# Kernel tuning notes

Measured on AMD Instinct MI355X. Metric: run time of the kernel, lower is better.

## Reference

```python
import jax, jax.numpy as jnp
import numpy as np

B, N, C, H = 2, 2048, 1024, 16
D = C // H
SCALE = 1.0 / np.sqrt(D)
MASK_VAL = -10000.0


def setup_inputs() -> dict:
    key = jax.random.key(0)
    k1, k2, k3 = jax.random.split(key, 3)
    hidden_state = jax.random.normal(k1, (B, N, C), dtype=jnp.float32)
    attention_mask = jax.random.randint(k2, (B, N), 0, 2) == 1  # True = padded
    # fused QKV projection weight, torch Linear convention: y = x @ W.T, W: [3C, C]
    W = jax.random.normal(k3, (3 * C, C), dtype=jnp.float32) * 0.02
    return {"hidden_state": hidden_state, "W": W, "attention_mask": attention_mask}


def reference(hidden_state, W, attention_mask):
    b, n, c = hidden_state.shape
    # fused QKV: [B,N,3C] -> [B,N,3,H,D] -> [3,B,H,N,D]
    wx = jnp.einsum('bnc,oc->bno', hidden_state, W).reshape(b, n, 3, H, D)
    wx = jnp.transpose(wx, (2, 0, 3, 1, 4))
    q, k, v = wx[0], wx[1], wx[2]
    scores = jnp.einsum('bhid,bhjd->bhij', q, k) * SCALE
    # construct_mask: pairwise OR of per-token padding mask, broadcast over heads
    m = attention_mask
    expanded = (m[:, None, :, None] | m[:, None, None, :])  # [B,1,N,N]
    scores = jnp.where(expanded, MASK_VAL, scores)
    scores = scores - jnp.max(scores, axis=-1, keepdims=True)
    att_weights = jax.nn.softmax(scores, axis=-1)
    # dropout_rate = 0.0 -> identity
    att = jnp.einsum('bhij,bhjd->bhid', att_weights, v)
    att = jnp.transpose(att, (0, 2, 1, 3)).reshape(b, n, c)
    return (att, att_weights)
```

## Files before the change

kernel.cpp:

```cpp
#include <hip/hip_runtime.h>


typedef unsigned short u16;
typedef __attribute__((ext_vector_type(8))) short bf16x8;
typedef __attribute__((ext_vector_type(4))) float f32x4;

#define B_ 2
#define N_ 2048
#define H_ 16
#define D_ 64
#define QKV_MAT 4194304
#define ATTW_OFF 4194304
#define OFF_MASK 25165824
#define OFF_FLAG 25182208
#define OFF_XB   25182464
#define OFF_WB   33571072

#define SCALE_L2 0.18033688011112042f
#define MASK_L2  -14426.950408889634f

__device__ __forceinline__ u16 f32_bf16(float f) {
  unsigned u = __float_as_uint(f);
  u += 0x7fffu + ((u >> 16) & 1u);
  return (u16)(u >> 16);
}
__device__ __forceinline__ float bf16_f32(unsigned h) {
  return __uint_as_float(h << 16);
}
__device__ __forceinline__ bf16x8 ld_frag(const u16* p) { return *(const bf16x8*)p; }

__device__ __forceinline__ void gld16(u16* l, const u16* g) {
  __builtin_amdgcn_global_load_lds(
      (const __attribute__((address_space(1))) void*)g,
      (__attribute__((address_space(3))) void*)l, 16, 0, 0);
}

__device__ __forceinline__ void bar_lgkm0() {
  __builtin_amdgcn_sched_barrier(0);
  asm volatile("s_waitcnt lgkmcnt(0)" ::: "memory");
  __builtin_amdgcn_s_barrier();
  __builtin_amdgcn_sched_barrier(0);
}
__device__ __forceinline__ void bar_vm4() {
  __builtin_amdgcn_sched_barrier(0);
  asm volatile("s_waitcnt vmcnt(4)" ::: "memory");
  __builtin_amdgcn_s_barrier();
  __builtin_amdgcn_sched_barrier(0);
}
__device__ __forceinline__ void bar_vm8() {
  __builtin_amdgcn_sched_barrier(0);
  asm volatile("s_waitcnt vmcnt(8)" ::: "memory");
  __builtin_amdgcn_s_barrier();
  __builtin_amdgcn_sched_barrier(0);
}

__global__ void detect_prep(const unsigned char* __restrict__ mraw,
                            const unsigned* __restrict__ X32,
                            int* __restrict__ flag) {
  __shared__ int votes, mflags;
  const int tid = threadIdx.x;
  if (tid == 0) { votes = 0; mflags = 0; }
  __syncthreads();
  int v = 0;
  for (int i = tid; i < 4096; i += 1024) {
    unsigned low = X32[i] & 0xFFFFu;
    unsigned e = (low >> 7) & 0xFFu;
    if (low == 0 || (e >= 80 && e <= 150)) v++;
  }
  atomicAdd(&votes, v);
  int fl = 0;
  for (int p = tid; p < B_ * N_; p += 1024) {
    unsigned char c = mraw[p];
    if (c > 1) fl |= 1;
    if (c && (p & 3) == 1) fl |= 4;
    if (c && (p & 3) != 0) fl |= 2;
    if (c && (p & 7) == 4) fl |= 8;
  }
  if (fl) atomicOr(&mflags, fl);
  __syncthreads();
  if (tid == 0) { flag[0] = (votes < 2600) ? 1 : 0; flag[1] = mflags; }
}

__global__ __launch_bounds__(256) void convert_in(const void* __restrict__ X,
                                                  const void* __restrict__ W,
                                                  const unsigned char* __restrict__ mraw,
                                                  u16* __restrict__ Xb, u16* __restrict__ Wb,
                                                  int* __restrict__ mout,
                                                  const int* __restrict__ flag) {
  const int f32m = flag[0];
  const int f = flag[1];
  const int gid = blockIdx.x * 256 + threadIdx.x;
  for (int i = gid; i < B_ * N_; i += gridDim.x * 256) {
    int m;
    if (f & 1) {
      if (f & 4) m = (((const u16*)mraw)[i] & 0x7FFFu) != 0;
      else       m = (((const unsigned*)mraw)[i] << 1) != 0;
    } else if (f & 2) m = mraw[i] != 0;
    else if (f & 8)   m = ((const int*)mraw)[i] != 0;
    else              m = ((const long long*)mraw)[i] != 0;
    mout[i] = m;
  }
  const int XC = (B_ * N_ * 1024) / 8;
  const int WC = (3072 * 1024) / 8;
  for (int idx = gid; idx < XC + WC; idx += gridDim.x * 256) {
    const void* src; u16* dst; int c;
    if (idx < XC) { c = idx; src = X; dst = Xb; }
    else          { c = idx - XC; src = W; dst = Wb; }
    if (f32m) {
      const float4* s = (const float4*)src;
      float4 a = s[c * 2], b = s[c * 2 + 1];
      unsigned p0 = (unsigned)f32_bf16(a.x) | ((unsigned)f32_bf16(a.y) << 16);
      unsigned p1 = (unsigned)f32_bf16(a.z) | ((unsigned)f32_bf16(a.w) << 16);
      unsigned p2 = (unsigned)f32_bf16(b.x) | ((unsigned)f32_bf16(b.y) << 16);
      unsigned p3 = (unsigned)f32_bf16(b.z) | ((unsigned)f32_bf16(b.w) << 16);
      ((uint4*)dst)[c] = make_uint4(p0, p1, p2, p3);
    } else {
      ((uint4*)dst)[c] = ((const uint4*)src)[c];
    }
  }
}

__global__ __launch_bounds__(256) void qkv_gemm(const u16* __restrict__ X,
                                                const u16* __restrict__ W,
                                                u16* __restrict__ qkv) {
  __shared__ u16 xs[128 * 64];
  __shared__ u16 wsh[128 * 64];
  const int tid = threadIdx.x;
  const int w = tid >> 6, l = tid & 63, quad = l >> 4, ln = l & 15;
  const int r0 = blockIdx.y * 128;
  const int o0 = blockIdx.x * 128;

  const f32x4 z4 = {0.f, 0.f, 0.f, 0.f};
  f32x4 acc[2][8];
#pragma unroll
  for (int rt = 0; rt < 2; rt++)
#pragma unroll
    for (int ct = 0; ct < 8; ct++) acc[rt][ct] = z4;

  for (int kc = 0; kc < 1024; kc += 64) {
#pragma unroll
    for (int ro = 0; ro < 4; ro++) {
      int q = ro * 256 + tid;
      int r = q >> 3, s = q & 7;
      int c = s ^ (r & 7);
      gld16(xs + q * 8, X + (size_t)(r0 + r) * 1024 + kc + c * 8);
      gld16(wsh + q * 8, W + (size_t)(o0 + r) * 1024 + kc + c * 8);
    }
    __syncthreads();
#pragma unroll
    for (int k2 = 0; k2 < 2; k2++) {
      bf16x8 af[2], bfr[8];
#pragma unroll
      for (int rt = 0; rt < 2; rt++) {
        int row = w * 32 + rt * 16 + ln;
        int slot = (k2 * 4 + quad) ^ (row & 7);
        af[rt] = ld_frag(xs + row * 64 + slot * 8);
      }
#pragma unroll
      for (int ct = 0; ct < 8; ct++) {
        int row = ct * 16 + ln;
        int slot = (k2 * 4 + quad) ^ (row & 7);
        bfr[ct] = ld_frag(wsh + row * 64 + slot * 8);
      }
#pragma unroll
      for (int rt = 0; rt < 2; rt++)
#pragma unroll
        for (int ct = 0; ct < 8; ct++)
          acc[rt][ct] = __builtin_amdgcn_mfma_f32_16x16x32_bf16(af[rt], bfr[ct], acc[rt][ct], 0, 0, 0);
    }
    __syncthreads();
  }

  const int b = r0 >> 11;
#pragma unroll
  for (int rt = 0; rt < 2; rt++) {
#pragma unroll
    for (int ct = 0; ct < 8; ct++) {
      int o = o0 + ct * 16 + ln;
      int sel = o >> 10;
      int h = (o >> 6) & 15;
      int d = o & 63;
      int nbase = (r0 & 2047) + w * 32 + rt * 16 + quad * 4;
      if (sel < 2) {
        size_t base = (size_t)sel * QKV_MAT + ((size_t)(b * 16 + h) * N_ + nbase) * D_ + d;
#pragma unroll
        for (int g = 0; g < 4; g++)
          qkv[base + (size_t)g * D_] = f32_bf16(acc[rt][ct][g]);
      } else {
        size_t base = 2 * (size_t)QKV_MAT + ((size_t)(b * 16 + h) * D_ + d) * N_ + nbase;
        unsigned lo = (unsigned)f32_bf16(acc[rt][ct][0]) | ((unsigned)f32_bf16(acc[rt][ct][1]) << 16);
        unsigned hi = (unsigned)f32_bf16(acc[rt][ct][2]) | ((unsigned)f32_bf16(acc[rt][ct][3]) << 16);
        *(uint2*)(qkv + base) = make_uint2(lo, hi);
      }
    }
  }
}

__global__ __launch_bounds__(256) void attn_kernel(const u16* __restrict__ qkv,
                                                   const int* __restrict__ mask,
                                                   void* __restrict__ outv,
                                                   const int* __restrict__ flag) {
  __shared__ u16 qs[128 * 64];
  __shared__ u16 ks[2][64 * 64];
  __shared__ u16 vs[2][64 * 64];
  __shared__ u16 ps[128 * 72];
  __shared__ float mrow[128];
  __shared__ float rlrow[128];

  const int of32 = __builtin_amdgcn_readfirstlane(flag[0]);
  u16* outh = (u16*)outv;
  float* outf = (float*)outv;

  const int tid = threadIdx.x;
  const int w = tid >> 6, l = tid & 63, quad = l >> 4, ln = l & 15;
  const int bh = blockIdx.x & 31;
  const int qt = blockIdx.x >> 5;
  const int b = bh >> 4, h = bh & 15;
  const int q0 = qt * 128;

  const u16* Qg = qkv + ((size_t)bh * N_ + q0) * D_;
  const u16* Kg = qkv + QKV_MAT + (size_t)bh * N_ * D_;
  const u16* Vg = qkv + 2 * (size_t)QKV_MAT + (size_t)bh * D_ * N_;
  const int* mb = mask + b * N_;
  const size_t attw_base = (size_t)ATTW_OFF + (size_t)bh * N_ * N_ + (size_t)q0 * N_;

#pragma unroll
  for (int ro = 0; ro < 4; ro++) {
    int q = ro * 256 + tid;
    int r = q >> 3, s = q & 7;
    int c = s ^ (r & 7);
    gld16(qs + q * 8, Qg + (size_t)r * D_ + c * 8);
  }
#pragma unroll
  for (int ro = 0; ro < 2; ro++) {
    int q = ro * 256 + tid;
    int r = q >> 3, s = q & 7;
    int c = s ^ (r & 7);
    gld16(ks[0] + q * 8, Kg + (size_t)r * D_ + c * 8);
  }
  int rowpad[2][4];
#pragma unroll
  for (int rt = 0; rt < 2; rt++)
#pragma unroll
    for (int g = 0; g < 4; g++)
      rowpad[rt][g] = mb[q0 + w * 32 + rt * 16 + quad * 4 + g];
  __syncthreads();

  bf16x8 qa[2][2];
#pragma unroll
  for (int rt = 0; rt < 2; rt++)
#pragma unroll
    for (int k2 = 0; k2 < 2; k2++) {
      int row = w * 32 + rt * 16 + ln;
      int slot = (k2 * 4 + quad) ^ (row & 7);
      qa[rt][k2] = ld_frag(qs + row * 64 + slot * 8);
    }

  float lsum[2][4] = {{0.f, 0.f, 0.f, 0.f}, {0.f, 0.f, 0.f, 0.f}};
  const f32x4 z4 = {0.f, 0.f, 0.f, 0.f};

  for (int kt = 0; kt < 32; kt++) {
    const int cur = kt & 1;
    if (kt < 31) {
#pragma unroll
      for (int ro = 0; ro < 2; ro++) {
        int q = ro * 256 + tid;
        int r = q >> 3, s = q & 7;
        int c = s ^ (r & 7);
        gld16(ks[cur ^ 1] + q * 8, Kg + (size_t)((kt + 1) * 64 + r) * D_ + c * 8);
      }
    }
    int cp[4];
#pragma unroll
    for (int ct = 0; ct < 4; ct++) cp[ct] = mb[kt * 64 + ct * 16 + ln];

    f32x4 sacc[2][4];
#pragma unroll
    for (int rt = 0; rt < 2; rt++)
#pragma unroll
      for (int ct = 0; ct < 4; ct++) sacc[rt][ct] = z4;
#pragma unroll
    for (int k2 = 0; k2 < 2; k2++) {
      bf16x8 kb[4];
#pragma unroll
      for (int ct = 0; ct < 4; ct++) {
        int row = ct * 16 + ln;
        int slot = (k2 * 4 + quad) ^ (row & 7);
        kb[ct] = ld_frag(ks[cur] + row * 64 + slot * 8);
      }
#pragma unroll
      for (int rt = 0; rt < 2; rt++)
#pragma unroll
        for (int ct = 0; ct < 4; ct++)
          sacc[rt][ct] = __builtin_amdgcn_mfma_f32_16x16x32_bf16(qa[rt][k2], kb[ct], sacc[rt][ct], 0, 0, 0);
    }
#pragma unroll
    for (int rt = 0; rt < 2; rt++)
#pragma unroll
      for (int g = 0; g < 4; g++) {
        float e = 0.f;
#pragma unroll
        for (int ct = 0; ct < 4; ct++) {
          float sv = sacc[rt][ct][g] * SCALE_L2;
          sv = (rowpad[rt][g] | cp[ct]) ? MASK_L2 : sv;
          e += __builtin_amdgcn_exp2f(sv);
        }
        lsum[rt][g] += e;
      }
    __syncthreads();
  }

#pragma unroll
  for (int ro = 0; ro < 2; ro++) {
    int q = ro * 256 + tid;
    int r = q >> 3, s = q & 7;
    int c = s ^ (r & 7);
    gld16(ks[0] + q * 8, Kg + (size_t)r * D_ + c * 8);
    gld16(vs[0] + q * 8, Vg + (size_t)r * N_ + c * 8);
  }

#pragma unroll
  for (int rt = 0; rt < 2; rt++)
#pragma unroll
    for (int g = 0; g < 4; g++) {
      float lv = lsum[rt][g];
      lv += __shfl_xor(lv, 1);
      lv += __shfl_xor(lv, 2);
      lv += __shfl_xor(lv, 4);
      lv += __shfl_xor(lv, 8);
      if (ln == 0) {
        int i = w * 32 + rt * 16 + quad * 4 + g;
        mrow[i] = rowpad[rt][g] ? MASK_L2 : 0.f;
        rlrow[i] = rowpad[rt][g] ? (1.f / 2048.f) : (1.f / lv);
      }
    }
  __syncthreads();

  bf16x8 qb[8][2];
  float mi[8], rli[8];
#pragma unroll
  for (int it = 0; it < 8; it++) {
    int row = it * 16 + ln;
#pragma unroll
    for (int k2 = 0; k2 < 2; k2++) {
      int slot = (k2 * 4 + quad) ^ (row & 7);
      qb[it][k2] = ld_frag(qs + row * 64 + slot * 8);
    }
    mi[it] = mrow[row];
    rli[it] = rlrow[row];
  }

  f32x4 oacc[2][4];
#pragma unroll
  for (int rt = 0; rt < 2; rt++)
#pragma unroll
    for (int dt = 0; dt < 4; dt++) oacc[rt][dt] = z4;

  for (int kt = 0; kt < 32; kt++) {
    const int cur = kt & 1;
    int cpj[4];
#pragma unroll
    for (int g = 0; g < 4; g++) cpj[g] = mb[kt * 64 + w * 16 + quad * 4 + g];

    bf16x8 ka[2];
#pragma unroll
    for (int k2 = 0; k2 < 2; k2++) {
      int row = w * 16 + ln;
      int slot = (k2 * 4 + quad) ^ (row & 7);
      ka[k2] = ld_frag(ks[cur] + row * 64 + slot * 8);
    }
#pragma unroll
    for (int it = 0; it < 8; it++) {
      f32x4 st = z4;
      st = __builtin_amdgcn_mfma_f32_16x16x32_bf16(ka[0], qb[it][0], st, 0, 0, 0);
      st = __builtin_amdgcn_mfma_f32_16x16x32_bf16(ka[1], qb[it][1], st, 0, 0, 0);
      bool rp = mi[it] < -5000.f;
      unsigned pk[4];
#pragma unroll
      for (int g = 0; g < 4; g++) {
        float sv = st[g] * SCALE_L2;
        sv = (cpj[g] || rp) ? MASK_L2 : sv;
        float p = __builtin_amdgcn_exp2f(sv - mi[it]) * rli[it];
        pk[g] = f32_bf16(p);
      }
      int iRow = it * 16 + ln;
      int jc = w * 16 + quad * 4;
      *(uint2*)(ps + iRow * 72 + jc) = make_uint2(pk[0] | (pk[1] << 16), pk[2] | (pk[3] << 16));
    }
    bar_lgkm0();

    if (kt < 31) {
#pragma unroll
      for (int ro = 0; ro < 2; ro++) {
        int q = ro * 256 + tid;
        int r = q >> 3, s = q & 7;
        int c = s ^ (r & 7);
        gld16(ks[cur ^ 1] + q * 8, Kg + (size_t)((kt + 1) * 64 + r) * D_ + c * 8);
        gld16(vs[cur ^ 1] + q * 8, Vg + (size_t)r * N_ + (kt + 1) * 64 + c * 8);
      }
    }

    if (!of32) {
#pragma unroll
      for (int ro = 0; ro < 4; ro++) {
        int q = ro * 256 + tid;
        int r = q >> 3, c = q & 7;
        uint4 v = *(const uint4*)(ps + r * 72 + c * 8);
        *(uint4*)(outh + attw_base + (size_t)r * N_ + kt * 64 + c * 8) = v;
      }
    } else {
#pragma unroll
      for (int ro = 0; ro < 8; ro++) {
        int q = ro * 256 + tid;
        int r = q >> 4, c4 = q & 15;
        uint2 v = *(const uint2*)(ps + r * 72 + c4 * 4);
        float4 o = make_float4(bf16_f32(v.x & 0xFFFFu), bf16_f32(v.x >> 16),
                               bf16_f32(v.y & 0xFFFFu), bf16_f32(v.y >> 16));
        *(float4*)(outf + attw_base + (size_t)r * N_ + kt * 64 + c4 * 4) = o;
      }
    }
#pragma unroll
    for (int k2 = 0; k2 < 2; k2++) {
      bf16x8 pa[2], vb[4];
#pragma unroll
      for (int rt = 0; rt < 2; rt++) {
        int row = w * 32 + rt * 16 + ln;
        pa[rt] = ld_frag(ps + row * 72 + k2 * 32 + quad * 8);
      }
#pragma unroll
      for (int dt = 0; dt < 4; dt++) {
        int row = dt * 16 + ln;
        int slot = (k2 * 4 + quad) ^ (row & 7);
        vb[dt] = ld_frag(vs[cur] + row * 64 + slot * 8);
      }
#pragma unroll
      for (int rt = 0; rt < 2; rt++)
#pragma unroll
        for (int dt = 0; dt < 4; dt++)
          oacc[rt][dt] = __builtin_amdgcn_mfma_f32_16x16x32_bf16(pa[rt], vb[dt], oacc[rt][dt], 0, 0, 0);
    }
    if (!of32) bar_vm4(); else bar_vm8();
  }

#pragma unroll
  for (int rt = 0; rt < 2; rt++)
#pragma unroll
    for (int dt = 0; dt < 4; dt++) {
      int d = dt * 16 + ln;
#pragma unroll
      for (int g = 0; g < 4; g++) {
        int i = w * 32 + rt * 16 + quad * 4 + g;
        size_t off = (size_t)(b * N_ + q0 + i) * 1024 + h * 64 + d;
        if (!of32) outh[off] = f32_bf16(oacc[rt][dt][g]);
        else       outf[off] = oacc[rt][dt][g];
      }
    }
}

extern "C" void kernel_launch(void* const* d_in, const int* in_sizes, int n_in,
                              void* d_out, int out_size, void* d_ws, size_t ws_size,
                              hipStream_t stream) {
  (void)in_sizes; (void)n_in; (void)out_size; (void)ws_size;
  const unsigned char* mraw = (const unsigned char*)d_in[2];
  char* ws = (char*)d_ws;
  u16* qkvws = (u16*)ws;
  int* maskws = (int*)(ws + OFF_MASK);
  int* flagws = (int*)(ws + OFF_FLAG);
  u16* Xb = (u16*)(ws + OFF_XB);
  u16* Wb = (u16*)(ws + OFF_WB);

  detect_prep<<<1, 1024, 0, stream>>>(mraw, (const unsigned*)d_in[0], flagws);
  convert_in<<<1792, 256, 0, stream>>>(d_in[0], d_in[1], mraw, Xb, Wb, maskws, flagws);
  qkv_gemm<<<dim3(24, 32), 256, 0, stream>>>(Xb, Wb, qkvws);
  attn_kernel<<<512, 256, 0, stream>>>(qkvws, maskws, d_out, flagws);
}
```

Measured before the change: 694.7 us.

## Split attention block across eight waves with 512 threads

New measurement: 730.2 us. 1.05x slower.

```diff
diff --git a/kernel.cpp b/kernel.cpp
--- a/kernel.cpp
+++ b/kernel.cpp
@@ -41,15 +41,15 @@
   __builtin_amdgcn_s_barrier();
   __builtin_amdgcn_sched_barrier(0);
 }
+__device__ __forceinline__ void bar_vm2() {
+  __builtin_amdgcn_sched_barrier(0);
+  asm volatile("s_waitcnt vmcnt(2)" ::: "memory");
+  __builtin_amdgcn_s_barrier();
+  __builtin_amdgcn_sched_barrier(0);
+}
 __device__ __forceinline__ void bar_vm4() {
   __builtin_amdgcn_sched_barrier(0);
   asm volatile("s_waitcnt vmcnt(4)" ::: "memory");
-  __builtin_amdgcn_s_barrier();
-  __builtin_amdgcn_sched_barrier(0);
-}
-__device__ __forceinline__ void bar_vm8() {
-  __builtin_amdgcn_sched_barrier(0);
-  asm volatile("s_waitcnt vmcnt(8)" ::: "memory");
   __builtin_amdgcn_s_barrier();
   __builtin_amdgcn_sched_barrier(0);
 }
@@ -196,10 +196,10 @@
   }
 }
 
-__global__ __launch_bounds__(256) void attn_kernel(const u16* __restrict__ qkv,
-                                                   const int* __restrict__ mask,
-                                                   void* __restrict__ outv,
-                                                   const int* __restrict__ flag) {
+__global__ __launch_bounds__(512, 4) void attn_kernel(const u16* __restrict__ qkv,
+                                                      const int* __restrict__ mask,
+                                                      void* __restrict__ outv,
+                                                      const int* __restrict__ flag) {
   __shared__ u16 qs[128 * 64];
   __shared__ u16 ks[2][64 * 64];
   __shared__ u16 vs[2][64 * 64];
@@ -212,11 +212,14 @@
   float* outf = (float*)outv;
 
   const int tid = threadIdx.x;
-  const int w = tid >> 6, l = tid & 63, quad = l >> 4, ln = l & 15;
+  const int w = tid >> 6;
+  const int l = tid & 63, quad = l >> 4, ln = l & 15;
   const int bh = blockIdx.x & 31;
   const int qt = blockIdx.x >> 5;
   const int b = bh >> 4, h = bh & 15;
   const int q0 = qt * 128;
+  const int jstrip = (w & 3) * 16;
+  const int baseit = (w >> 2) * 4;
 
   const u16* Qg = qkv + ((size_t)bh * N_ + q0) * D_;
   const u16* Kg = qkv + QKV_MAT + (size_t)bh * N_ * D_;
@@ -225,60 +228,50 @@
   const size_t attw_base = (size_t)ATTW_OFF + (size_t)bh * N_ * N_ + (size_t)q0 * N_;
 
 #pragma unroll
-  for (int ro = 0; ro < 4; ro++) {
-    int q = ro * 256 + tid;
+  for (int ro = 0; ro < 2; ro++) {
+    int q = ro * 512 + tid;
     int r = q >> 3, s = q & 7;
     int c = s ^ (r & 7);
     gld16(qs + q * 8, Qg + (size_t)r * D_ + c * 8);
   }
-#pragma unroll
-  for (int ro = 0; ro < 2; ro++) {
-    int q = ro * 256 + tid;
+  {
+    int q = tid;
     int r = q >> 3, s = q & 7;
     int c = s ^ (r & 7);
     gld16(ks[0] + q * 8, Kg + (size_t)r * D_ + c * 8);
   }
-  int rowpad[2][4];
-#pragma unroll
-  for (int rt = 0; rt < 2; rt++)
-#pragma unroll
-    for (int g = 0; g < 4; g++)
-      rowpad[rt][g] = mb[q0 + w * 32 + rt * 16 + quad * 4 + g];
+  int rowpad[4];
+#pragma unroll
+  for (int g = 0; g < 4; g++)
+    rowpad[g] = mb[q0 + w * 16 + quad * 4 + g];
   __syncthreads();
 
-  bf16x8 qa[2][2];
-#pragma unroll
-  for (int rt = 0; rt < 2; rt++)
-#pragma unroll
-    for (int k2 = 0; k2 < 2; k2++) {
-      int row = w * 32 + rt * 16 + ln;
-      int slot = (k2 * 4 + quad) ^ (row & 7);
-      qa[rt][k2] = ld_frag(qs + row * 64 + slot * 8);
-    }
-
-  float lsum[2][4] = {{0.f, 0.f, 0.f, 0.f}, {0.f, 0.f, 0.f, 0.f}};
+  bf16x8 qa[2];
+#pragma unroll
+  for (int k2 = 0; k2 < 2; k2++) {
+    int row = w * 16 + ln;
+    int slot = (k2 * 4 + quad) ^ (row & 7);
+    qa[k2] = ld_frag(qs + row * 64 + slot * 8);
+  }
+
+  float lsum[4] = {0.f, 0.f, 0.f, 0.f};
   const f32x4 z4 = {0.f, 0.f, 0.f, 0.f};
 
   for (int kt = 0; kt < 32; kt++) {
     const int cur = kt & 1;
     if (kt < 31) {
-#pragma unroll
-      for (int ro = 0; ro < 2; ro++) {
-        int q = ro * 256 + tid;
-        int r = q >> 3, s = q & 7;
-        int c = s ^ (r & 7);
-        gld16(ks[cur ^ 1] + q * 8, Kg + (size_t)((kt + 1) * 64 + r) * D_ + c * 8);
-      }
+      int q = tid;
+      int r = q >> 3, s = q & 7;
+      int c = s ^ (r & 7);
+      gld16(ks[cur ^ 1] + q * 8, Kg + (size_t)((kt + 1) * 64 + r) * D_ + c * 8);
     }
     int cp[4];
 #pragma unroll
     for (int ct = 0; ct < 4; ct++) cp[ct] = mb[kt * 64 + ct * 16 + ln];
 
-    f32x4 sacc[2][4];
-#pragma unroll
-    for (int rt = 0; rt < 2; rt++)
-#pragma unroll
-      for (int ct = 0; ct < 4; ct++) sacc[rt][ct] = z4;
+    f32x4 sacc[4];
+#pragma unroll
+    for (int ct = 0; ct < 4; ct++) sacc[ct] = z4;
 #pragma unroll
     for (int k2 = 0; k2 < 2; k2++) {
       bf16x8 kb[4];
@@ -289,30 +282,25 @@
         kb[ct] = ld_frag(ks[cur] + row * 64 + slot * 8);
       }
 #pragma unroll
-      for (int rt = 0; rt < 2; rt++)
-#pragma unroll
-        for (int ct = 0; ct < 4; ct++)
-          sacc[rt][ct] = __builtin_amdgcn_mfma_f32_16x16x32_bf16(qa[rt][k2], kb[ct], sacc[rt][ct], 0, 0, 0);
-    }
-#pragma unroll
-    for (int rt = 0; rt < 2; rt++)
-#pragma unroll
-      for (int g = 0; g < 4; g++) {
-        float e = 0.f;
-#pragma unroll
-        for (int ct = 0; ct < 4; ct++) {
-          float sv = sacc[rt][ct][g] * SCALE_L2;
-          sv = (rowpad[rt][g] | cp[ct]) ? MASK_L2 : sv;
-          e += __builtin_amdgcn_exp2f(sv);
-        }
-        lsum[rt][g] += e;
-      }
+      for (int ct = 0; ct < 4; ct++)
+        sacc[ct] = __builtin_amdgcn_mfma_f32_16x16x32_bf16(qa[k2], kb[ct], sacc[ct], 0, 0, 0);
+    }
+#pragma unroll
+    for (int g = 0; g < 4; g++) {
+      float e = 0.f;
+#pragma unroll
+      for (int ct = 0; ct < 4; ct++) {
+        float sv = sacc[ct][g] * SCALE_L2;
+        sv = (rowpad[g] | cp[ct]) ? MASK_L2 : sv;
+        e += __builtin_amdgcn_exp2f(sv);
+      }
+      lsum[g] += e;
+    }
     __syncthreads();
   }
 
-#pragma unroll
-  for (int ro = 0; ro < 2; ro++) {
-    int q = ro * 256 + tid;
+  {
+    int q = tid;
     int r = q >> 3, s = q & 7;
     int c = s ^ (r & 7);
     gld16(ks[0] + q * 8, Kg + (size_t)r * D_ + c * 8);
@@ -320,98 +308,91 @@
   }
 
 #pragma unroll
-  for (int rt = 0; rt < 2; rt++)
-#pragma unroll
-    for (int g = 0; g < 4; g++) {
-      float lv = lsum[rt][g];
-      lv += __shfl_xor(lv, 1);
-      lv += __shfl_xor(lv, 2);
-      lv += __shfl_xor(lv, 4);
-      lv += __shfl_xor(lv, 8);
-      if (ln == 0) {
-        int i = w * 32 + rt * 16 + quad * 4 + g;
-        mrow[i] = rowpad[rt][g] ? MASK_L2 : 0.f;
-        rlrow[i] = rowpad[rt][g] ? (1.f / 2048.f) : (1.f / lv);
-      }
-    }
+  for (int g = 0; g < 4; g++) {
+    float lv = lsum[g];
+    lv += __shfl_xor(lv, 1);
+    lv += __shfl_xor(lv, 2);
+    lv += __shfl_xor(lv, 4);
+    lv += __shfl_xor(lv, 8);
+    if (ln == 0) {
+      int i = w * 16 + quad * 4 + g;
+      mrow[i] = rowpad[g] ? MASK_L2 : 0.f;
+      rlrow[i] = rowpad[g] ? (1.f / 2048.f) : (1.f / lv);
+    }
+  }
   __syncthreads();
 
-  bf16x8 qb[8][2];
-  float mi[8], rli[8];
-#pragma unroll
-  for (int it = 0; it < 8; it++) {
-    int row = it * 16 + ln;
+  bf16x8 qb[4][2];
+  float mi[4], rli[4];
+#pragma unroll
+  for (int itl = 0; itl < 4; itl++) {
+    int row = (baseit + itl) * 16 + ln;
 #pragma unroll
     for (int k2 = 0; k2 < 2; k2++) {
       int slot = (k2 * 4 + quad) ^ (row & 7);
-      qb[it][k2] = ld_frag(qs + row * 64 + slot * 8);
-    }
-    mi[it] = mrow[row];
-    rli[it] = rlrow[row];
-  }
-
-  f32x4 oacc[2][4];
-#pragma unroll
-  for (int rt = 0; rt < 2; rt++)
-#pragma unroll
-    for (int dt = 0; dt < 4; dt++) oacc[rt][dt] = z4;
+      qb[itl][k2] = ld_frag(qs + row * 64 + slot * 8);
+    }
+    mi[itl] = mrow[row];
+    rli[itl] = rlrow[row];
+  }
+
+  f32x4 oacc[4];
+#pragma unroll
+  for (int dt = 0; dt < 4; dt++) oacc[dt] = z4;
 
   for (int kt = 0; kt < 32; kt++) {
     const int cur = kt & 1;
     int cpj[4];
 #pragma unroll
-    for (int g = 0; g < 4; g++) cpj[g] = mb[kt * 64 + w * 16 + quad * 4 + g];
+    for (int g = 0; g < 4; g++) cpj[g] = mb[kt * 64 + jstrip + quad * 4 + g];
 
     bf16x8 ka[2];
 #pragma unroll
     for (int k2 = 0; k2 < 2; k2++) {
-      int row = w * 16 + ln;
+      int row = jstrip + ln;
       int slot = (k2 * 4 + quad) ^ (row & 7);
       ka[k2] = ld_frag(ks[cur] + row * 64 + slot * 8);
     }
 #pragma unroll
-    for (int it = 0; it < 8; it++) {
+    for (int itl = 0; itl < 4; itl++) {
       f32x4 st = z4;
-      st = __builtin_amdgcn_mfma_f32_16x16x32_bf16(ka[0], qb[it][0], st, 0, 0, 0);
-      st = __builtin_amdgcn_mfma_f32_16x16x32_bf16(ka[1], qb[it][1], st, 0, 0, 0);
-      bool rp = mi[it] < -5000.f;
+      st = __builtin_amdgcn_mfma_f32_16x16x32_bf16(ka[0], qb[itl][0], st, 0, 0, 0);
+      st = __builtin_amdgcn_mfma_f32_16x16x32_bf16(ka[1], qb[itl][1], st, 0, 0, 0);
+      bool rp = mi[itl] < -5000.f;
       unsigned pk[4];
 #pragma unroll
       for (int g = 0; g < 4; g++) {
         float sv = st[g] * SCALE_L2;
         sv = (cpj[g] || rp) ? MASK_L2 : sv;
-        float p = __builtin_amdgcn_exp2f(sv - mi[it]) * rli[it];
+        float p = __builtin_amdgcn_exp2f(sv - mi[itl]) * rli[itl];
         pk[g] = f32_bf16(p);
       }
-      int iRow = it * 16 + ln;
-      int jc = w * 16 + quad * 4;
+      int iRow = (baseit + itl) * 16 + ln;
+      int jc = jstrip + quad * 4;
       *(uint2*)(ps + iRow * 72 + jc) = make_uint2(pk[0] | (pk[1] << 16), pk[2] | (pk[3] << 16));
     }
     bar_lgkm0();
 
     if (kt < 31) {
+      int q = tid;
+      int r = q >> 3, s = q & 7;
+      int c = s ^ (r & 7);
+      gld16(ks[cur ^ 1] + q * 8, Kg + (size_t)((kt + 1) * 64 + r) * D_ + c * 8);
+      gld16(vs[cur ^ 1] + q * 8, Vg + (size_t)r * N_ + (kt + 1) * 64 + c * 8);
+    }
+
+    if (!of32) {
 #pragma unroll
       for (int ro = 0; ro < 2; ro++) {
-        int q = ro * 256 + tid;
-        int r = q >> 3, s = q & 7;
-        int c = s ^ (r & 7);
-        gld16(ks[cur ^ 1] + q * 8, Kg + (size_t)((kt + 1) * 64 + r) * D_ + c * 8);
-        gld16(vs[cur ^ 1] + q * 8, Vg + (size_t)r * N_ + (kt + 1) * 64 + c * 8);
-      }
-    }
-
-    if (!of32) {
-#pragma unroll
-      for (int ro = 0; ro < 4; ro++) {
-        int q = ro * 256 + tid;
+        int q = ro * 512 + tid;
         int r = q >> 3, c = q & 7;
         uint4 v = *(const uint4*)(ps + r * 72 + c * 8);
         *(uint4*)(outh + attw_base + (size_t)r * N_ + kt * 64 + c * 8) = v;
       }
     } else {
 #pragma unroll
-      for (int ro = 0; ro < 8; ro++) {
-        int q = ro * 256 + tid;
+      for (int ro = 0; ro < 4; ro++) {
+        int q = ro * 512 + tid;
         int r = q >> 4, c4 = q & 15;
         uint2 v = *(const uint2*)(ps + r * 72 + c4 * 4);
         float4 o = make_float4(bf16_f32(v.x & 0xFFFFu), bf16_f32(v.x >> 16),
@@ -421,11 +402,10 @@
     }
 #pragma unroll
     for (int k2 = 0; k2 < 2; k2++) {
-      bf16x8 pa[2], vb[4];
-#pragma unroll
-      for (int rt = 0; rt < 2; rt++) {
-        int row = w * 32 + rt * 16 + ln;
-        pa[rt] = ld_frag(ps + row * 72 + k2 * 32 + quad * 8);
+      bf16x8 pa, vb[4];
+      {
+        int row = w * 16 + ln;
+        pa = ld_frag(ps + row * 72 + k2 * 32 + quad * 8);
       }
 #pragma unroll
       for (int dt = 0; dt < 4; dt++) {
@@ -434,27 +414,23 @@
         vb[dt] = ld_frag(vs[cur] + row * 64 + slot * 8);
       }
 #pragma unroll
-      for (int rt = 0; rt < 2; rt++)
-#pragma unroll
-        for (int dt = 0; dt < 4; dt++)
-          oacc[rt][dt] = __builtin_amdgcn_mfma_f32_16x16x32_bf16(pa[rt], vb[dt], oacc[rt][dt], 0, 0, 0);
-    }
-    if (!of32) bar_vm4(); else bar_vm8();
-  }
-
-#pragma unroll
-  for (int rt = 0; rt < 2; rt++)
-#pragma unroll
-    for (int dt = 0; dt < 4; dt++) {
-      int d = dt * 16 + ln;
-#pragma unroll
-      for (int g = 0; g < 4; g++) {
-        int i = w * 32 + rt * 16 + quad * 4 + g;
-        size_t off = (size_t)(b * N_ + q0 + i) * 1024 + h * 64 + d;
-        if (!of32) outh[off] = f32_bf16(oacc[rt][dt][g]);
-        else       outf[off] = oacc[rt][dt][g];
-      }
-    }
+      for (int dt = 0; dt < 4; dt++)
+        oacc[dt] = __builtin_amdgcn_mfma_f32_16x16x32_bf16(pa, vb[dt], oacc[dt], 0, 0, 0);
+    }
+    if (!of32) bar_vm2(); else bar_vm4();
+  }
+
+#pragma unroll
+  for (int dt = 0; dt < 4; dt++) {
+    int d = dt * 16 + ln;
+#pragma unroll
+    for (int g = 0; g < 4; g++) {
+      int i = w * 16 + quad * 4 + g;
+      size_t off = (size_t)(b * N_ + q0 + i) * 1024 + h * 64 + d;
+      if (!of32) outh[off] = f32_bf16(oacc[dt][g]);
+      else       outf[off] = oacc[dt][g];
+    }
+  }
 }
 
 extern "C" void kernel_launch(void* const* d_in, const int* in_sizes, int n_in,
@@ -472,5 +448,5 @@
   detect_prep<<<1, 1024, 0, stream>>>(mraw, (const unsigned*)d_in[0], flagws);
   convert_in<<<1792, 256, 0, stream>>>(d_in[0], d_in[1], mraw, Xb, Wb, maskws, flagws);
   qkv_gemm<<<dim3(24, 32), 256, 0, stream>>>(Xb, Wb, qkvws);
-  attn_kernel<<<512, 256, 0, stream>>>(qkvws, maskws, d_out, flagws);
-}
+  attn_kernel<<<512, 512, 0, stream>>>(qkvws, maskws, d_out, flagws);
+}
```

## Write attention weights directly from registers and cache padding mask in LDS

Applied to the files above, without the earlier changes.

Result: no change. 695.6 us (+0.1%).

```diff
diff --git a/kernel.cpp b/kernel.cpp
--- a/kernel.cpp
+++ b/kernel.cpp
@@ -41,15 +41,9 @@
   __builtin_amdgcn_s_barrier();
   __builtin_amdgcn_sched_barrier(0);
 }
-__device__ __forceinline__ void bar_vm4() {
+__device__ __forceinline__ void bar_vm8_lgkm0() {
   __builtin_amdgcn_sched_barrier(0);
-  asm volatile("s_waitcnt vmcnt(4)" ::: "memory");
-  __builtin_amdgcn_s_barrier();
-  __builtin_amdgcn_sched_barrier(0);
-}
-__device__ __forceinline__ void bar_vm8() {
-  __builtin_amdgcn_sched_barrier(0);
-  asm volatile("s_waitcnt vmcnt(8)" ::: "memory");
+  asm volatile("s_waitcnt vmcnt(8) lgkmcnt(0)" ::: "memory");
   __builtin_amdgcn_s_barrier();
   __builtin_amdgcn_sched_barrier(0);
 }
@@ -204,6 +198,7 @@
   __shared__ u16 ks[2][64 * 64];
   __shared__ u16 vs[2][64 * 64];
   __shared__ u16 ps[128 * 72];
+  __shared__ u16 msk[2048];
   __shared__ float mrow[128];
   __shared__ float rlrow[128];
 
@@ -238,6 +233,8 @@
     int c = s ^ (r & 7);
     gld16(ks[0] + q * 8, Kg + (size_t)r * D_ + c * 8);
   }
+#pragma unroll
+  for (int i = tid; i < 2048; i += 256) msk[i] = (u16)mb[i];
   int rowpad[2][4];
 #pragma unroll
   for (int rt = 0; rt < 2; rt++)
@@ -272,7 +269,7 @@
     }
     int cp[4];
 #pragma unroll
-    for (int ct = 0; ct < 4; ct++) cp[ct] = mb[kt * 64 + ct * 16 + ln];
+    for (int ct = 0; ct < 4; ct++) cp[ct] = msk[kt * 64 + ct * 16 + ln];
 
     f32x4 sacc[2][4];
 #pragma unroll
@@ -358,37 +355,6 @@
 
   for (int kt = 0; kt < 32; kt++) {
     const int cur = kt & 1;
-    int cpj[4];
-#pragma unroll
-    for (int g = 0; g < 4; g++) cpj[g] = mb[kt * 64 + w * 16 + quad * 4 + g];
-
-    bf16x8 ka[2];
-#pragma unroll
-    for (int k2 = 0; k2 < 2; k2++) {
-      int row = w * 16 + ln;
-      int slot = (k2 * 4 + quad) ^ (row & 7);
-      ka[k2] = ld_frag(ks[cur] + row * 64 + slot * 8);
-    }
-#pragma unroll
-    for (int it = 0; it < 8; it++) {
-      f32x4 st = z4;
-      st = __builtin_amdgcn_mfma_f32_16x16x32_bf16(ka[0], qb[it][0], st, 0, 0, 0);
-      st = __builtin_amdgcn_mfma_f32_16x16x32_bf16(ka[1], qb[it][1], st, 0, 0, 0);
-      bool rp = mi[it] < -5000.f;
-      unsigned pk[4];
-#pragma unroll
-      for (int g = 0; g < 4; g++) {
-        float sv = st[g] * SCALE_L2;
-        sv = (cpj[g] || rp) ? MASK_L2 : sv;
-        float p = __builtin_amdgcn_exp2f(sv - mi[it]) * rli[it];
-        pk[g] = f32_bf16(p);
-      }
-      int iRow = it * 16 + ln;
-      int jc = w * 16 + quad * 4;
-      *(uint2*)(ps + iRow * 72 + jc) = make_uint2(pk[0] | (pk[1] << 16), pk[2] | (pk[3] << 16));
-    }
-    bar_lgkm0();
-
     if (kt < 31) {
 #pragma unroll
       for (int ro = 0; ro < 2; ro++) {
@@ -399,26 +365,41 @@
         gld16(vs[cur ^ 1] + q * 8, Vg + (size_t)r * N_ + (kt + 1) * 64 + c * 8);
       }
     }
-
-    if (!of32) {
-#pragma unroll
-      for (int ro = 0; ro < 4; ro++) {
-        int q = ro * 256 + tid;
-        int r = q >> 3, c = q & 7;
-        uint4 v = *(const uint4*)(ps + r * 72 + c * 8);
-        *(uint4*)(outh + attw_base + (size_t)r * N_ + kt * 64 + c * 8) = v;
-      }
-    } else {
-#pragma unroll
-      for (int ro = 0; ro < 8; ro++) {
-        int q = ro * 256 + tid;
-        int r = q >> 4, c4 = q & 15;
-        uint2 v = *(const uint2*)(ps + r * 72 + c4 * 4);
-        float4 o = make_float4(bf16_f32(v.x & 0xFFFFu), bf16_f32(v.x >> 16),
-                               bf16_f32(v.y & 0xFFFFu), bf16_f32(v.y >> 16));
-        *(float4*)(outf + attw_base + (size_t)r * N_ + kt * 64 + c4 * 4) = o;
-      }
-    }
+    int cpj[4];
+#pragma unroll
+    for (int g = 0; g < 4; g++) cpj[g] = msk[kt * 64 + w * 16 + quad * 4 + g];
+
+    bf16x8 ka[2];
+#pragma unroll
+    for (int k2 = 0; k2 < 2; k2++) {
+      int row = w * 16 + ln;
+      int slot = (k2 * 4 + quad) ^ (row & 7);
+      ka[k2] = ld_frag(ks[cur] + row * 64 + slot * 8);
+    }
+#pragma unroll
+    for (int it = 0; it < 8; it++) {
+      f32x4 st = z4;
+      st = __builtin_amdgcn_mfma_f32_16x16x32_bf16(ka[0], qb[it][0], st, 0, 0, 0);
+      st = __builtin_amdgcn_mfma_f32_16x16x32_bf16(ka[1], qb[it][1], st, 0, 0, 0);
+      bool rp = mi[it] < -5000.f;
+      float p[4];
+      unsigned pk[4];
+#pragma unroll
+      for (int g = 0; g < 4; g++) {
+        float sv = st[g] * SCALE_L2;
+        sv = (cpj[g] || rp) ? MASK_L2 : sv;
+        p[g] = __builtin_amdgcn_exp2f(sv - mi[it]) * rli[it];
+        pk[g] = f32_bf16(p[g]);
+      }
+      int iRow = it * 16 + ln;
+      int jc = w * 16 + quad * 4;
+      size_t goff = attw_base + (size_t)iRow * N_ + kt * 64 + jc;
+      if (!of32) *(uint2*)(outh + goff) = make_uint2(pk[0] | (pk[1] << 16), pk[2] | (pk[3] << 16));
+      else       *(float4*)(outf + goff) = make_float4(p[0], p[1], p[2], p[3]);
+      *(uint2*)(ps + iRow * 72 + jc) = make_uint2(pk[0] | (pk[1] << 16), pk[2] | (pk[3] << 16));
+    }
+    bar_lgkm0();
+
 #pragma unroll
     for (int k2 = 0; k2 < 2; k2++) {
       bf16x8 pa[2], vb[4];
@@ -439,7 +420,7 @@
         for (int dt = 0; dt < 4; dt++)
           oacc[rt][dt] = __builtin_amdgcn_mfma_f32_16x16x32_bf16(pa[rt], vb[dt], oacc[rt][dt], 0, 0, 0);
     }
-    if (!of32) bar_vm4(); else bar_vm8();
+    bar_vm8_lgkm0();
   }
 
 #pragma unroll
```
